# Performance work log

Hardware: AMD Instinct MI355X
Metric: run time of the kernel (lower is better)

## Reference

```python
import jax, jax.numpy as jnp
import numpy as np

N, T, D, H = 256, 512, 256, 256


def setup_inputs() -> dict:
    key = jax.random.key(0)
    ks = jax.random.split(key, 9)
    scale_x = float(np.sqrt(6.0 / (D + H)))  # xavier_uniform range approx
    scale_h = float(np.sqrt(6.0 / (H + H)))
    def wx(k):
        return jax.random.uniform(k, (D, H), jnp.float32, -scale_x, scale_x)
    def wh(k):
        return jax.random.uniform(k, (H, H), jnp.float32, -scale_h, scale_h)
    inp = {
        'x': jax.random.normal(ks[0], (N, T, D), jnp.float32),
        'w_ii': wx(ks[1]), 'w_hi': wh(ks[2]),
        'w_if': wx(ks[3]), 'w_hf': wh(ks[4]),
        'w_ig': wx(ks[5]), 'w_hg': wh(ks[6]),
        'w_io': wx(ks[7]), 'w_ho': wh(ks[8]),
        # init_hidden() zeros all 1-D params
        'b_ii': jnp.zeros((H,), jnp.float32), 'b_hi': jnp.zeros((H,), jnp.float32),
        'b_if': jnp.zeros((H,), jnp.float32), 'b_hf': jnp.zeros((H,), jnp.float32),
        'b_ig': jnp.zeros((H,), jnp.float32), 'b_hg': jnp.zeros((H,), jnp.float32),
        'b_io': jnp.zeros((H,), jnp.float32), 'b_ho': jnp.zeros((H,), jnp.float32),
    }
    return inp


def reference(x, w_ii, w_hi, w_if, w_hf, w_ig, w_hg, w_io, w_ho,
              b_ii, b_hi, b_if, b_hf, b_ig, b_hg, b_io, b_ho):
    # Fuse the 4 input projections and 4 hidden projections into 2 GEMMs
    # (mathematically identical to the 8 separate matmuls).
    Wx = jnp.concatenate([w_ii, w_if, w_ig, w_io], axis=1)  # (D, 4H)
    Wh = jnp.concatenate([w_hi, w_hf, w_hg, w_ho], axis=1)  # (H, 4H)
    b = jnp.concatenate([b_ii + b_hi, b_if + b_hf, b_ig + b_hg, b_io + b_ho])  # (4H,)
    n, t, _ = x.shape
    h = x.shape[2]  # noqa (not used)
    # Precompute input projections for all timesteps: (T, N, 4H)
    xW = jnp.einsum('ntd,dg->tng', x, Wx)
    h0 = jnp.zeros((n, w_hi.shape[0]), x.dtype)
    c0 = jnp.zeros_like(h0)

    def step(carry, xw_t):
        h_t, c_t = carry
        gates = xw_t + h_t @ Wh + b  # (N, 4H)
        i_t, f_t, g_t, o_t = jnp.split(gates, 4, axis=1)
        i_t = jax.nn.sigmoid(i_t)
        f_t = jax.nn.sigmoid(f_t)
        g_t = jnp.tanh(g_t)
        o_t = jax.nn.sigmoid(o_t)
        c_t = f_t * c_t + i_t * g_t
        h_t = o_t * jnp.tanh(c_t)
        return (h_t, c_t), None

    (h_T, c_T), _ = jax.lax.scan(step, (h0, c0), xW)
    return (h_T, c_T)
```

## Files before the change

### kernel.cpp

```cpp
#include <hip/hip_runtime.h>
#include <cstdint>

typedef float  f32x4  __attribute__((ext_vector_type(4)));
typedef __bf16 bf16x8 __attribute__((ext_vector_type(8)));
typedef int    i32x4  __attribute__((ext_vector_type(4)));
typedef unsigned short u16;
typedef u16 u16x4 __attribute__((ext_vector_type(4)));

#define TT 512

__device__ __forceinline__ u16 f2bf(float f) {
  unsigned u = __builtin_bit_cast(unsigned, f);
  unsigned r = u + 0x7fffu + ((u >> 16) & 1u);
  return (u16)(r >> 16);
}
__device__ __forceinline__ float bflo(unsigned d) { return __builtin_bit_cast(float, d << 16); }
__device__ __forceinline__ float bfhi(unsigned d) { return __builtin_bit_cast(float, d & 0xffff0000u); }
__device__ __forceinline__ float rcpf(float x) { return __builtin_amdgcn_rcpf(x); }
__device__ __forceinline__ float fsig(float x) { return rcpf(1.f + __expf(-x)); }
__device__ __forceinline__ float ftanh(float x) { return 1.f - 2.f * rcpf(1.f + __expf(2.f * x)); }
__device__ __forceinline__ void gload_lds16(const u16* g, u16* l) {
  __builtin_amdgcn_global_load_lds((const __attribute__((address_space(1))) void*)(g),
                                   (__attribute__((address_space(3))) void*)(l), 16, 0, 0);
}

__global__ __launch_bounds__(256) void prep_x(const float* __restrict__ x, u16* __restrict__ xb) {
  long o = ((long)blockIdx.x * 256 + threadIdx.x) * 4;
  int d = (int)(o & 255);
  int n = (int)((o >> 8) & 255);
  int t = (int)(o >> 16);
  const float4 v = *(const float4*)(x + ((long)n << 17) + ((long)t << 8) + d);
  u16x4 p;
  p[0] = f2bf(v.x); p[1] = f2bf(v.y); p[2] = f2bf(v.z); p[3] = f2bf(v.w);
  *(u16x4*)(xb + o) = p;
}

__global__ __launch_bounds__(256) void prep_w(
    const float* __restrict__ wii, const float* __restrict__ whi,
    const float* __restrict__ wif, const float* __restrict__ whf,
    const float* __restrict__ wig, const float* __restrict__ whg,
    const float* __restrict__ wio, const float* __restrict__ who,
    const float* __restrict__ bii, const float* __restrict__ bhi,
    const float* __restrict__ bif, const float* __restrict__ bhf,
    const float* __restrict__ big_, const float* __restrict__ bhg,
    const float* __restrict__ bio, const float* __restrict__ bho,
    u16* __restrict__ Wxb, signed char* __restrict__ Whq,
    float* __restrict__ wscale, float* __restrict__ bsum) {
  __shared__ float red[256];
  int b = blockIdx.x;
  int tid = threadIdx.x;
  if (b < 1024) {
    const float* wx[4] = {wii, wif, wig, wio};
    int G = b >> 8, h = b & 255;
    Wxb[b * 256 + tid] = f2bf(wx[G][tid * 256 + h]);
  } else if (b < 2048) {
    const float* wh[4] = {whi, whf, whg, who};
    int cidx = b - 1024;
    int G = cidx >> 8, h = cidx & 255;
    float w = wh[G][tid * 256 + h];
    red[tid] = fabsf(w);
    __syncthreads();
    for (int s = 128; s > 0; s >>= 1) {
      if (tid < s) red[tid] = fmaxf(red[tid], red[tid + s]);
      __syncthreads();
    }
    float mx = red[0];
    float scale = (mx > 0.f) ? mx * (1.f / 127.f) : 1.f;
    float qf = rintf(w / scale);
    qf = fminf(127.f, fmaxf(-127.f, qf));
    Whq[cidx * 256 + tid] = (signed char)(int)qf;
    if (tid == 0) wscale[cidx] = scale * (1.f / 127.f);
  } else {
    const float* bx[4] = {bii, bif, big_, bio};
    const float* bh[4] = {bhi, bhf, bhg, bho};
    for (int G = 0; G < 4; ++G) bsum[G * 256 + tid] = bx[G][tid] + bh[G][tid];
  }
}

__global__ __launch_bounds__(256) void gemm_xw(const u16* __restrict__ A, const u16* __restrict__ Bt,
                                               const float* __restrict__ bias, u16* __restrict__ xWp) {
  __shared__ u16 As[128 * 32];
  __shared__ u16 Bs[128 * 32];
  int bid = blockIdx.x;
  int bm = bid & 1023, bn = bid >> 10;
  int tid = threadIdx.x;
  int l = tid & 63, w = tid >> 6;
  int wm = w >> 1, wn = w & 1;
  f32x4 acc[4][4];
#pragma unroll
  for (int i = 0; i < 4; ++i)
#pragma unroll
    for (int j = 0; j < 4; ++j) acc[i][j] = (f32x4){0.f, 0.f, 0.f, 0.f};

  const u16* Ab = A + (size_t)bm * 128 * 256;
  const u16* Bb = Bt + (size_t)bn * 128 * 256;
  int row = tid >> 2;
  int ch = tid & 3;
  for (int ko = 0; ko < 8; ++ko) {
    __syncthreads();
    gload_lds16(Ab + (size_t)row * 256 + ko * 32 + ch * 8, As + tid * 8);
    gload_lds16(Ab + (size_t)(row + 64) * 256 + ko * 32 + ch * 8, As + 2048 + tid * 8);
    gload_lds16(Bb + (size_t)row * 256 + ko * 32 + ch * 8, Bs + tid * 8);
    gload_lds16(Bb + (size_t)(row + 64) * 256 + ko * 32 + ch * 8, Bs + 2048 + tid * 8);
    __syncthreads();
    bf16x8 af[4], bfr[4];
#pragma unroll
    for (int mt = 0; mt < 4; ++mt)
      af[mt] = *reinterpret_cast<const bf16x8*>(As + (wm * 64 + mt * 16 + (l & 15)) * 32 + (l >> 4) * 8);
#pragma unroll
    for (int nt = 0; nt < 4; ++nt)
      bfr[nt] = *reinterpret_cast<const bf16x8*>(Bs + (wn * 64 + nt * 16 + (l & 15)) * 32 + (l >> 4) * 8);
#pragma unroll
    for (int mt = 0; mt < 4; ++mt)
#pragma unroll
      for (int nt = 0; nt < 4; ++nt)
        acc[mt][nt] = __builtin_amdgcn_mfma_f32_16x16x32_bf16(af[mt], bfr[nt], acc[mt][nt], 0, 0, 0);
  }
#pragma unroll
  for (int mt = 0; mt < 4; ++mt) {
    int tm = bm * 8 + wm * 4 + mt;
#pragma unroll
    for (int nt = 0; nt < 4; ++nt) {
      int tn = bn * 8 + wn * 4 + nt;
      float bv = bias[tn * 16 + (l & 15)];
      u16x4 pk;
#pragma unroll
      for (int r = 0; r < 4; ++r) pk[r] = f2bf(acc[mt][nt][r] + bv);
      *reinterpret_cast<u16x4*>(xWp + ((size_t)(tm * 64 + tn) * 256 + l * 4)) = pk;
    }
  }
}

__global__ __launch_bounds__(512, 2) void lstm_rec(const signed char* __restrict__ Whq,
                                                   const float* __restrict__ wscale,
                                                   const u16* __restrict__ xWp,
                                                   float* __restrict__ out) {
  __shared__ __align__(16) signed char hb[2][576];
  int p = blockIdx.x;
  int xcd = p & 7, q8 = (p >> 3) & 7, tsel = p >> 6;
  int G = xcd * 2 + tsel;
  int tid = threadIdx.x;
  int wid = tid >> 6, l = tid & 63;
  int c = l & 15, q = (l >> 4) & 3;
  int tt = q >> 1, rsel = q & 1;

  for (int i = tid; i < 288; i += 512) ((int*)hb)[i] = 0;

  i32x4 bw[4][2][4];
#pragma unroll
  for (int g = 0; g < 4; ++g)
#pragma unroll
    for (int ttl = 0; ttl < 2; ++ttl) {
      int col = g * 256 + wid * 32 + ttl * 16 + c;
#pragma unroll
      for (int ks = 0; ks < 4; ++ks)
        bw[g][ttl][ks] = *reinterpret_cast<const i32x4*>(Whq + (size_t)col * 256 + ks * 64 + q * 16);
    }
  float sc8[4];
#pragma unroll
  for (int g = 0; g < 4; ++g) sc8[g] = wscale[g * 256 + wid * 32 + tt * 16 + c];

  const char* xbase = (const char*)xWp + (size_t)G * 32768;
  int xoff[4];
#pragma unroll
  for (int g = 0; g < 4; ++g) {
    int tn = g * 16 + wid * 2 + tt;
    xoff[g] = tn * 512 + (((q8 >> 1) * 16 + c) * 8) + (q8 & 1) * 4;
  }
  unsigned xw0[4], xw1[4];
#pragma unroll
  for (int g = 0; g < 4; ++g) xw0[g] = *(const unsigned*)(xbase + xoff[g]);
  xbase += 524288;

  i32x4 zacc = (i32x4){0, 0, 0, 0};
  float cs = 0.f, hh = 0.f;
  __syncthreads();

#define STEP(CUR, XW_CUR, XW_NXT)                                               \
  {                                                                             \
    _Pragma("unroll")                                                           \
    for (int g = 0; g < 4; ++g) XW_NXT[g] = *(const unsigned*)(xbase + xoff[g]);\
    const signed char* hr = hb[CUR ^ 1];                                        \
    i32x4 acc[4][2];                                                            \
    {                                                                           \
      i32x4 a0 = *(const i32x4*)(hr + (c & 1) * 288 + q * 16);                  \
      _Pragma("unroll")                                                         \
      for (int g = 0; g < 4; ++g) {                                             \
        __asm__("v_mfma_i32_16x16x64_i8 %0, %1, %2, %3"                         \
                : "=&v"(acc[g][0]) : "v"(a0), "a"(bw[g][0][0]), "v"(zacc));     \
        __asm__("v_mfma_i32_16x16x64_i8 %0, %1, %2, %3"                         \
                : "=&v"(acc[g][1]) : "v"(a0), "a"(bw[g][1][0]), "v"(zacc));     \
      }                                                                         \
    }                                                                           \
    _Pragma("unroll")                                                           \
    for (int ks = 1; ks < 4; ++ks) {                                            \
      i32x4 a = *(const i32x4*)(hr + (c & 1) * 288 + ks * 64 + q * 16);         \
      _Pragma("unroll")                                                         \
      for (int g = 0; g < 4; ++g) {                                             \
        __asm__("v_mfma_i32_16x16x64_i8 %0, %1, %2, %0"                         \
                : "+v"(acc[g][0]) : "v"(a), "a"(bw[g][0][ks]));                 \
        __asm__("v_mfma_i32_16x16x64_i8 %0, %1, %2, %0"                         \
                : "+v"(acc[g][1]) : "v"(a), "a"(bw[g][1][ks]));                 \
      }                                                                         \
    }                                                                           \
    __asm__ volatile("s_nop 7\n\ts_nop 7\n\ts_nop 7");   \
    float a4[4];                                                                \
    _Pragma("unroll")                                                           \
    for (int g = 0; g < 4; ++g) {                                               \
      int e = tt ? (rsel ? acc[g][1][1] : acc[g][1][0])                         \
                 : (rsel ? acc[g][0][1] : acc[g][0][0]);                        \
      unsigned d = XW_CUR[g];                                                   \
      float xv = rsel ? bfhi(d) : bflo(d);                                      \
      a4[g] = (float)e * sc8[g] + xv;                                           \
    }                                                                           \
    float gi = fsig(a4[0]);                                                     \
    float gf = fsig(a4[1]);                                                     \
    float gg = ftanh(a4[2]);                                                    \
    float go = fsig(a4[3]);                                                     \
    cs = gf * cs + gi * gg;                                                     \
    hh = go * ftanh(cs);                                                        \
    int hq = (int)rintf(hh * 127.f);                                            \
    hb[CUR][rsel * 288 + wid * 32 + tt * 16 + c] = (signed char)hq;             \
    xbase += 524288;                                                            \
    __builtin_amdgcn_s_waitcnt(0xC07F);   \
    __builtin_amdgcn_s_barrier();                                               \
  }

  for (int t = 0; t < TT; t += 2) {
    STEP(0, xw0, xw1)
    STEP(1, xw1, xw0)
  }
#undef STEP

  {
    int n = G * 16 + q8 * 2 + rsel;
    int hu = wid * 32 + tt * 16 + c;
    out[(size_t)n * 256 + hu] = hh;
    out[65536 + (size_t)n * 256 + hu] = cs;
  }
}

extern "C" void kernel_launch(void* const* d_in, const int* in_sizes, int n_in,
                              void* d_out, int out_size, void* d_ws, size_t ws_size,
                              hipStream_t stream) {
  const float* x   = (const float*)d_in[0];
  const float* wii = (const float*)d_in[1];
  const float* whi = (const float*)d_in[2];
  const float* wif = (const float*)d_in[3];
  const float* whf = (const float*)d_in[4];
  const float* wig = (const float*)d_in[5];
  const float* whg = (const float*)d_in[6];
  const float* wio = (const float*)d_in[7];
  const float* who = (const float*)d_in[8];
  const float* bii = (const float*)d_in[9];
  const float* bhi = (const float*)d_in[10];
  const float* bif = (const float*)d_in[11];
  const float* bhf = (const float*)d_in[12];
  const float* big_ = (const float*)d_in[13];
  const float* bhg = (const float*)d_in[14];
  const float* bio = (const float*)d_in[15];
  const float* bho = (const float*)d_in[16];

  char* ws = (char*)d_ws;
  u16*   xb     = (u16*)(ws);
  u16*   Wxb    = (u16*)(ws + 67108864);
  signed char* Whq = (signed char*)(ws + 67633152);
  float* wscale = (float*)(ws + 67895296);
  float* bsum   = (float*)(ws + 67899392);
  u16*   xWp    = (u16*)(ws + 67903488);
  float* out = (float*)d_out;

  prep_x<<<32768, 256, 0, stream>>>(x, xb);
  prep_w<<<2049, 256, 0, stream>>>(wii, whi, wif, whf, wig, whg, wio, who,
                                   bii, bhi, bif, bhf, big_, bhg, bio, bho,
                                   Wxb, Whq, wscale, bsum);
  gemm_xw<<<8192, 256, 0, stream>>>(xb, Wxb, bsum, xWp);
  lstm_rec<<<128, 512, 0, stream>>>(Whq, wscale, xWp, out);
}
```

Measured before the change: 746.4 us.

## Fuse input-projection GEMM with LSTM recurrence via flag-synchronized producer blocks

Replaces the separate input-projection GEMM and recurrence kernels with one cooperative kernel of 256 blocks. 128 blocks run the recurrence while the other 128 compute the x·Wx projection timestep by timestep. Each producer publishes a per-timestep flag with a release fence, and consumers poll those flags before loading xW with atomic loads. The aim is to overlap the large GEMM with the latency-bound recurrence instead of running them back to back. The cost is polling overhead in the recurrent loop, and the change relies on co-residency of all blocks, which is why it uses a cooperative launch.

```diff
diff --git a/kernel.cpp b/kernel.cpp
--- a/kernel.cpp
+++ b/kernel.cpp
@@ -77,74 +77,84 @@
   }
 }
 
-__global__ __launch_bounds__(256) void gemm_xw(const u16* __restrict__ A, const u16* __restrict__ Bt,
-                                               const float* __restrict__ bias, u16* __restrict__ xWp) {
-  __shared__ u16 As[128 * 32];
-  __shared__ u16 Bs[128 * 32];
+__global__ __launch_bounds__(512, 2) void lstm_fused(
+    const u16* __restrict__ xb, const u16* __restrict__ Wxb,
+    const float* __restrict__ bsum,
+    const signed char* __restrict__ Whq, const float* __restrict__ wscale,
+    u16* __restrict__ xWp, unsigned* __restrict__ flags,
+    float* __restrict__ out) {
+  __shared__ __align__(16) char smem[24576];
   int bid = blockIdx.x;
-  int bm = bid & 1023, bn = bid >> 10;
+  int xcd = bid & 7;
+  int j = bid >> 3;
   int tid = threadIdx.x;
-  int l = tid & 63, w = tid >> 6;
-  int wm = w >> 1, wn = w & 1;
-  f32x4 acc[4][4];
-#pragma unroll
-  for (int i = 0; i < 4; ++i)
-#pragma unroll
-    for (int j = 0; j < 4; ++j) acc[i][j] = (f32x4){0.f, 0.f, 0.f, 0.f};
-
-  const u16* Ab = A + (size_t)bm * 128 * 256;
-  const u16* Bb = Bt + (size_t)bn * 128 * 256;
-  int row = tid >> 2;
-  int ch = tid & 3;
-  for (int ko = 0; ko < 8; ++ko) {
-    __syncthreads();
-    gload_lds16(Ab + (size_t)row * 256 + ko * 32 + ch * 8, As + tid * 8);
-    gload_lds16(Ab + (size_t)(row + 64) * 256 + ko * 32 + ch * 8, As + 2048 + tid * 8);
-    gload_lds16(Bb + (size_t)row * 256 + ko * 32 + ch * 8, Bs + tid * 8);
-    gload_lds16(Bb + (size_t)(row + 64) * 256 + ko * 32 + ch * 8, Bs + 2048 + tid * 8);
-    __syncthreads();
-    bf16x8 af[4], bfr[4];
-#pragma unroll
-    for (int mt = 0; mt < 4; ++mt)
-      af[mt] = *reinterpret_cast<const bf16x8*>(As + (wm * 64 + mt * 16 + (l & 15)) * 32 + (l >> 4) * 8);
-#pragma unroll
-    for (int nt = 0; nt < 4; ++nt)
-      bfr[nt] = *reinterpret_cast<const bf16x8*>(Bs + (wn * 64 + nt * 16 + (l & 15)) * 32 + (l >> 4) * 8);
-#pragma unroll
-    for (int mt = 0; mt < 4; ++mt)
-#pragma unroll
-      for (int nt = 0; nt < 4; ++nt)
-        acc[mt][nt] = __builtin_amdgcn_mfma_f32_16x16x32_bf16(af[mt], bfr[nt], acc[mt][nt], 0, 0, 0);
-  }
-#pragma unroll
-  for (int mt = 0; mt < 4; ++mt) {
-    int tm = bm * 8 + wm * 4 + mt;
-#pragma unroll
-    for (int nt = 0; nt < 4; ++nt) {
-      int tn = bn * 8 + wn * 4 + nt;
-      float bv = bias[tn * 16 + (l & 15)];
-      u16x4 pk;
-#pragma unroll
-      for (int r = 0; r < 4; ++r) pk[r] = f2bf(acc[mt][nt][r] + bv);
-      *reinterpret_cast<u16x4*>(xWp + ((size_t)(tm * 64 + tn) * 256 + l * 4)) = pk;
+  int l = tid & 63;
+
+  if (j >= 16) {
+    int toff = j - 16;
+    int n8 = xcd;
+    u16* As = (u16*)smem;
+    u16* Bs = (u16*)(smem + 16384);
+    const u16* Bb = Wxb + (size_t)n8 * 32768;
+    int row = tid >> 2, ch = tid & 3;
+    int w = tid >> 6, wm = w >> 1, wn = w & 1;
+    for (int it = 0; it < 32; ++it) {
+      int t = toff + (it << 4);
+      const u16* Ab = xb + (size_t)t * 65536;
+      f32x4 acc[4][4];
+#pragma unroll
+      for (int i = 0; i < 4; ++i)
+#pragma unroll
+        for (int jj = 0; jj < 4; ++jj) acc[i][jj] = (f32x4){0.f, 0.f, 0.f, 0.f};
+      for (int ko = 0; ko < 8; ++ko) {
+        __syncthreads();
+        gload_lds16(Ab + (size_t)row * 256 + ko * 32 + ch * 8, As + tid * 8);
+        gload_lds16(Ab + (size_t)(row + 128) * 256 + ko * 32 + ch * 8, As + 4096 + tid * 8);
+        gload_lds16(Bb + (size_t)row * 256 + ko * 32 + ch * 8, Bs + tid * 8);
+        __syncthreads();
+        bf16x8 bfr[4];
+#pragma unroll
+        for (int nt = 0; nt < 4; ++nt)
+          bfr[nt] = *reinterpret_cast<const bf16x8*>(Bs + (wn * 64 + nt * 16 + (l & 15)) * 32 + (l >> 4) * 8);
+#pragma unroll
+        for (int mt = 0; mt < 4; ++mt) {
+          bf16x8 af = *reinterpret_cast<const bf16x8*>(As + (wm * 64 + mt * 16 + (l & 15)) * 32 + (l >> 4) * 8);
+#pragma unroll
+          for (int nt = 0; nt < 4; ++nt)
+            acc[mt][nt] = __builtin_amdgcn_mfma_f32_16x16x32_bf16(af, bfr[nt], acc[mt][nt], 0, 0, 0);
+        }
+      }
+#pragma unroll
+      for (int mt = 0; mt < 4; ++mt) {
+        int tm = t * 16 + wm * 4 + mt;
+#pragma unroll
+        for (int nt = 0; nt < 4; ++nt) {
+          int tn = n8 * 8 + wn * 4 + nt;
+          float bv = bsum[tn * 16 + (l & 15)];
+          u16x4 pk;
+#pragma unroll
+          for (int r = 0; r < 4; ++r) pk[r] = f2bf(acc[mt][nt][r] + bv);
+          *reinterpret_cast<u16x4*>(xWp + ((size_t)(tm * 64 + tn) * 256 + l * 4)) = pk;
+        }
+      }
+      __syncthreads();
+      if (tid == 0) {
+        __builtin_amdgcn_fence(__ATOMIC_RELEASE, "agent");
+        __hip_atomic_store(flags + t * 8 + n8, 1u, __ATOMIC_RELAXED, __HIP_MEMORY_SCOPE_AGENT);
+      }
     }
-  }
-}
-
-__global__ __launch_bounds__(512, 2) void lstm_rec(const signed char* __restrict__ Whq,
-                                                   const float* __restrict__ wscale,
-                                                   const u16* __restrict__ xWp,
-                                                   float* __restrict__ out) {
-  __shared__ __align__(16) signed char hb[2][576];
-  int p = blockIdx.x;
-  int xcd = p & 7, q8 = (p >> 3) & 7, tsel = p >> 6;
+    return;
+  }
+
+  signed char* hb0 = (signed char*)smem;
+  signed char* hb1 = (signed char*)smem + 576;
+  int q8 = j & 7, tsel = j >> 3;
   int G = xcd * 2 + tsel;
-  int tid = threadIdx.x;
-  int wid = tid >> 6, l = tid & 63;
+  int wid = tid >> 6;
   int c = l & 15, q = (l >> 4) & 3;
   int tt = q >> 1, rsel = q & 1;
 
-  for (int i = tid; i < 288; i += 512) ((int*)hb)[i] = 0;
+  for (int i = tid; i < 288; i += 512) ((int*)smem)[i] = 0;
 
   i32x4 bw[4][2][4];
 #pragma unroll
@@ -167,20 +177,60 @@
     int tn = g * 16 + wid * 2 + tt;
     xoff[g] = tn * 512 + (((q8 >> 1) * 16 + c) * 8) + (q8 & 1) * 4;
   }
+
+  int Wv = -1;
+  unsigned pv = 0;
+  {
+    int guard = 0;
+    while (Wv < 1 && ++guard < 50000000) {
+      int td = Wv + 1 + (l >> 3);
+      int tdc = td <= 511 ? td : 511;
+      unsigned v = __hip_atomic_load(flags + tdc * 8 + (l & 7),
+                                     __ATOMIC_RELAXED, __HIP_MEMORY_SCOPE_AGENT);
+      if (td > 511) v = 1u;
+      if (__all((int)(v == 1u))) { Wv += 8; if (Wv > 511) Wv = 511; }
+    }
+  }
   unsigned xw0[4], xw1[4];
 #pragma unroll
-  for (int g = 0; g < 4; ++g) xw0[g] = *(const unsigned*)(xbase + xoff[g]);
+  for (int g = 0; g < 4; ++g)
+    xw0[g] = __hip_atomic_load((const unsigned*)(xbase + xoff[g]),
+                               __ATOMIC_RELAXED, __HIP_MEMORY_SCOPE_AGENT);
   xbase += 524288;
 
   i32x4 zacc = (i32x4){0, 0, 0, 0};
   float cs = 0.f, hh = 0.f;
   __syncthreads();
 
-#define STEP(CUR, XW_CUR, XW_NXT)                                               \
+#define STEP(CUR, XW_CUR, XW_NXT, TCUR)                                         \
   {                                                                             \
+    if (Wv < 511) {             \
+      if (__all((int)(pv == 1u))) { Wv += 8; if (Wv > 511) Wv = 511; }          \
+      if (Wv < 511) {                                                           \
+        int td = Wv + 1 + (l >> 3);                                             \
+        int tdc = td <= 511 ? td : 511;                                         \
+        unsigned v = __hip_atomic_load(flags + tdc * 8 + (l & 7),               \
+                        __ATOMIC_RELAXED, __HIP_MEMORY_SCOPE_AGENT);            \
+        pv = (td > 511) ? 1u : v;                                               \
+      }                                                                         \
+    }                                                                           \
+    if (Wv < (TCUR) + 1 && Wv < 511) {            \
+      int guard = 0;                                                            \
+      do {                                                                      \
+        int td = Wv + 1 + (l >> 3);                                             \
+        int tdc = td <= 511 ? td : 511;                                         \
+        unsigned v = __hip_atomic_load(flags + tdc * 8 + (l & 7),               \
+                        __ATOMIC_RELAXED, __HIP_MEMORY_SCOPE_AGENT);            \
+        if (td > 511) v = 1u;                                                   \
+        if (__all((int)(v == 1u))) { Wv += 8; if (Wv > 511) Wv = 511; }         \
+      } while (Wv < (TCUR) + 1 && Wv < 511 && ++guard < 20000000);              \
+      pv = 0u;                                                                  \
+    }                                                                           \
     _Pragma("unroll")                                                           \
-    for (int g = 0; g < 4; ++g) XW_NXT[g] = *(const unsigned*)(xbase + xoff[g]);\
-    const signed char* hr = hb[CUR ^ 1];                                        \
+    for (int g = 0; g < 4; ++g)                                                 \
+      XW_NXT[g] = __hip_atomic_load((const unsigned*)(xbase + xoff[g]),         \
+                      __ATOMIC_RELAXED, __HIP_MEMORY_SCOPE_AGENT);              \
+    const signed char* hr = (CUR) ? hb0 : hb1;                                  \
     i32x4 acc[4][2];                                                            \
     {                                                                           \
       i32x4 a0 = *(const i32x4*)(hr + (c & 1) * 288 + q * 16);                  \
@@ -220,15 +270,15 @@
     cs = gf * cs + gi * gg;                                                     \
     hh = go * ftanh(cs);                                                        \
     int hq = (int)rintf(hh * 127.f);                                            \
-    hb[CUR][rsel * 288 + wid * 32 + tt * 16 + c] = (signed char)hq;             \
+    ((CUR) ? hb1 : hb0)[rsel * 288 + wid * 32 + tt * 16 + c] = (signed char)hq; \
     xbase += 524288;                                                            \
     __builtin_amdgcn_s_waitcnt(0xC07F);   \
     __builtin_amdgcn_s_barrier();                                               \
   }
 
   for (int t = 0; t < TT; t += 2) {
-    STEP(0, xw0, xw1)
-    STEP(1, xw1, xw0)
+    STEP(0, xw0, xw1, t)
+    STEP(1, xw1, xw0, t + 1)
   }
 #undef STEP
 
@@ -267,13 +317,27 @@
   signed char* Whq = (signed char*)(ws + 67633152);
   float* wscale = (float*)(ws + 67895296);
   float* bsum   = (float*)(ws + 67899392);
-  u16*   xWp    = (u16*)(ws + 67903488);
+  unsigned* flags = (unsigned*)(ws + 67903488);
+  u16*   xWp    = (u16*)(ws + 67919872);
   float* out = (float*)d_out;
 
+  hipMemsetAsync(flags, 0, 16384, stream);
   prep_x<<<32768, 256, 0, stream>>>(x, xb);
   prep_w<<<2049, 256, 0, stream>>>(wii, whi, wif, whf, wig, whg, wio, who,
                                    bii, bhi, bif, bhf, big_, bhg, bio, bho,
                                    Wxb, Whq, wscale, bsum);
-  gemm_xw<<<8192, 256, 0, stream>>>(xb, Wxb, bsum, xWp);
-  lstm_rec<<<128, 512, 0, stream>>>(Whq, wscale, xWp, out);
-}
+
+  void* args[8];
+  const u16* xbA = xb; const u16* WxbA = Wxb; const float* bsumA = bsum;
+  const signed char* WhqA = Whq; const float* wscaleA = wscale;
+  u16* xWpA = xWp; unsigned* flagsA = flags; float* outA = (float*)d_out;
+  args[0] = (void*)&xbA;
+  args[1] = (void*)&WxbA;
+  args[2] = (void*)&bsumA;
+  args[3] = (void*)&WhqA;
+  args[4] = (void*)&wscaleA;
+  args[5] = (void*)&xWpA;
+  args[6] = (void*)&flagsA;
+  args[7] = (void*)&outA;
+  hipLaunchCooperativeKernel((const void*)lstm_fused, dim3(256), dim3(512), args, 0, stream);
+}
```

Result: slower. 887.9 us (+19.0%).
